# Performance work log

Measured on AMD Instinct MI355X. Metric: run time of the kernel, lower is better.

Reference implementation:

```python
import jax, jax.numpy as jnp
import numpy as np

NUM_LATENT = 1024
LATENT_DIM = 256
BETA = 0.25
N_TOKENS = 65536


def setup_inputs() -> dict:
    key = jax.random.key(0)
    k1, k2 = jax.random.split(key)
    latent_embedding = jax.random.normal(k1, (N_TOKENS, LATENT_DIM), dtype=jnp.float32)
    # torch.nn.init.uniform_(codebook, -1/num_latent, 1/num_latent)
    codebook = jax.random.uniform(
        k2, (NUM_LATENT, LATENT_DIM), dtype=jnp.float32,
        minval=-1.0 / NUM_LATENT, maxval=1.0 / NUM_LATENT)
    return {"latent_embedding": latent_embedding, "codebook": codebook}


def reference(latent_embedding, codebook):
    le_det = jax.lax.stop_gradient(latent_embedding)  # [N, D]
    # distances[n,k] = ||z_n||^2 + ||c_k||^2 - 2 z_n . c_k   (z detached, codebook NOT)
    distances = (jnp.sum(le_det ** 2, axis=1, keepdims=True)
                 + jnp.sum(codebook ** 2, axis=1)
                 - 2.0 * jnp.matmul(le_det, codebook.T))  # [N, K]
    encoding_inds = jnp.argmin(distances, axis=1)  # [N]
    # one_hot @ codebook == gather rows of codebook
    quantized_latents = codebook[encoding_inds]  # [N, D]
    num_latent = codebook.shape[0]
    commitment_loss = jnp.mean((jax.lax.stop_gradient(quantized_latents)
                                - latent_embedding) ** 2) * num_latent
    embedding_loss = jnp.mean((quantized_latents - le_det) ** 2) * num_latent
    vq_loss = embedding_loss + commitment_loss * BETA
    probs = jax.nn.softmax(-distances, axis=1)  # [N, K]
    probs = jnp.clip(jnp.mean(probs, axis=0, keepdims=True), 0.001, 0.999)  # [1, K]
    return (quantized_latents, codebook, probs, vq_loss)
```

## Files before the change

### kernel.cpp

```cpp
#include <hip/hip_runtime.h>

#define N_TOK 65536
#define DIM   256
#define K_CODES 1024
#define CB_OFF    16777216
#define PROBS_OFF (16777216 + 262144)
#define LOSS_OFF  (16777216 + 262144 + 1024)
#define TM 64

typedef float  f32x4  __attribute__((ext_vector_type(4)));
typedef short  s16x8  __attribute__((ext_vector_type(8)));

__device__ __forceinline__ unsigned short f32_to_bf16(float x) {
    unsigned u = __float_as_uint(x);
    unsigned r = (u + 0x7FFFu + ((u >> 16) & 1u)) >> 16;
    return (unsigned short)r;
}
__device__ __forceinline__ unsigned fkey(float a) {
    unsigned u = __float_as_uint(a);
    unsigned m = (unsigned)(((int)u) >> 31);
    return u ^ (m | 0x80000000u);
}
__device__ __forceinline__ float fkey_inv(unsigned k) {
    unsigned u = (k & 0x80000000u) ? (k ^ 0x80000000u) : ~k;
    return __uint_as_float(u);
}

__device__ __forceinline__ unsigned red16_max_u(unsigned v) {
    unsigned t;
    t = (unsigned)__builtin_amdgcn_update_dpp(0, (int)v, 0xB1,  0xF, 0xF, true); v = v > t ? v : t;
    t = (unsigned)__builtin_amdgcn_update_dpp(0, (int)v, 0x4E,  0xF, 0xF, true); v = v > t ? v : t;
    t = (unsigned)__builtin_amdgcn_update_dpp(0, (int)v, 0x141, 0xF, 0xF, true); v = v > t ? v : t;
    t = (unsigned)__builtin_amdgcn_update_dpp(0, (int)v, 0x140, 0xF, 0xF, true); v = v > t ? v : t;
    return v;
}
__device__ __forceinline__ float red16_sum_f(float v) {
    float t;
    t = __uint_as_float((unsigned)__builtin_amdgcn_update_dpp(0, (int)__float_as_uint(v), 0xB1,  0xF, 0xF, true)); v += t;
    t = __uint_as_float((unsigned)__builtin_amdgcn_update_dpp(0, (int)__float_as_uint(v), 0x4E,  0xF, 0xF, true)); v += t;
    t = __uint_as_float((unsigned)__builtin_amdgcn_update_dpp(0, (int)__float_as_uint(v), 0x141, 0xF, 0xF, true)); v += t;
    t = __uint_as_float((unsigned)__builtin_amdgcn_update_dpp(0, (int)__float_as_uint(v), 0x140, 0xF, 0xF, true)); v += t;
    return v;
}

__global__ __launch_bounds__(512) void k_prep(const float* __restrict__ cb,
                                              float* __restrict__ c2,
                                              unsigned short* __restrict__ cbf,
                                              float* __restrict__ probs_part,
                                              float* __restrict__ lossR,
                                              float* __restrict__ outcb,
                                              int zcount, int nloss, int docopy) {
    const int g  = blockIdx.x;
    const int t  = threadIdx.x;
    const int wv = t >> 6;
    const int ln = t & 63;
    const int l15 = ln & 15, q = ln >> 4;

    const float* zp = cb + (size_t)(g * 16 + l15) * DIM + wv * 32 + q * 8;
    f32x4 z0 = *(const f32x4*)(zp);
    f32x4 z1 = *(const f32x4*)(zp + 4);
    s16x8 a;
    a[0] = (short)f32_to_bf16(z0[0]); a[1] = (short)f32_to_bf16(z0[1]);
    a[2] = (short)f32_to_bf16(z0[2]); a[3] = (short)f32_to_bf16(z0[3]);
    a[4] = (short)f32_to_bf16(z1[0]); a[5] = (short)f32_to_bf16(z1[1]);
    a[6] = (short)f32_to_bf16(z1[2]); a[7] = (short)f32_to_bf16(z1[3]);
    *(s16x8*)(cbf + (size_t)(g * 8 + wv) * 1024 + ln * 8) = a;

    float s = z0[0]*z0[0] + z0[1]*z0[1] + z0[2]*z0[2] + z0[3]*z0[3]
            + z1[0]*z1[0] + z1[1]*z1[1] + z1[2]*z1[2] + z1[3]*z1[3];
    s += __shfl_xor(s, 16, 64);
    s += __shfl_xor(s, 32, 64);
    __shared__ float c2p[8][16];
    if (q == 0) c2p[wv][l15] = s;

    const int base = g * 512 + t;
    if (base < nloss) lossR[base] = 0.f;
    if (base < zcount) probs_part[base] = 0.f;
    if (base + 32768 < zcount) probs_part[base + 32768] = 0.f;
    if (docopy) {
        #pragma unroll
        for (int i = 0; i < 8; i++) outcb[base + i * 32768] = cb[base + i * 32768];
    }

    __syncthreads();
    if (t < 16) {
        float acc = 0.f;
        #pragma unroll
        for (int ww = 0; ww < 8; ww++) acc += c2p[ww][t];
        c2[g * 16 + t] = acc;
    }
}

__global__ __launch_bounds__(1024, 4) void k_main(const float* __restrict__ z,
                                                  const float* __restrict__ cb,
                                                  const unsigned short* __restrict__ cbf,
                                                  const float* __restrict__ c2,
                                                  float* __restrict__ out_q,
                                                  float* __restrict__ probs_part,
                                                  float* __restrict__ lossR,
                                                  int repmask) {
    const int t   = threadIdx.x;
    const int w   = t >> 6;
    const int ln  = t & 63;
    const int q   = ln >> 4;
    const int l15 = ln & 15;
    const int k0  = w * 64;
    const int n0  = blockIdx.x * TM;
    float* pp = probs_part +
        (size_t)((repmask < 0) ? (int)blockIdx.x : (int)(blockIdx.x & repmask)) * K_CODES;

    __shared__ unsigned short a_lds[32 * 64 * 8];
    __shared__ float    z2p[32][16];
    __shared__ unsigned kred[16][64];
    __shared__ float    ered[16][64];
    __shared__ int   fidx[64];
    __shared__ float fU[64];

    #pragma unroll
    for (int rep = 0; rep < 2; rep++) {
        const int f   = t + rep * 1024;
        const int md  = w + rep * 16;
        const int m   = md >> 3;
        const int dsv = md & 7;
        const int row = m * 16 + l15;
        const int dim = dsv * 32 + q * 8;
        const float* zp = z + (size_t)(n0 + row) * DIM + dim;
        f32x4 z0 = *(const f32x4*)(zp);
        f32x4 z1 = *(const f32x4*)(zp + 4);
        s16x8 a;
        a[0] = (short)f32_to_bf16(z0[0]); a[1] = (short)f32_to_bf16(z0[1]);
        a[2] = (short)f32_to_bf16(z0[2]); a[3] = (short)f32_to_bf16(z0[3]);
        a[4] = (short)f32_to_bf16(z1[0]); a[5] = (short)f32_to_bf16(z1[1]);
        a[6] = (short)f32_to_bf16(z1[2]); a[7] = (short)f32_to_bf16(z1[3]);
        *(s16x8*)(a_lds + (size_t)f * 8) = a;
        float s = z0[0]*z0[0] + z0[1]*z0[1] + z0[2]*z0[2] + z0[3]*z0[3]
                + z1[0]*z1[0] + z1[1]*z1[1] + z1[2]*z1[2] + z1[3]*z1[3];
        s += __shfl_xor(s, 16, 64);
        s += __shfl_xor(s, 32, 64);
        if (q == 0) z2p[md][l15] = s;
    }

    float c2v[4];
    #pragma unroll
    for (int nt = 0; nt < 4; nt++) c2v[nt] = c2[k0 + nt * 16 + l15];
    f32x4 acc[4][4];
    #pragma unroll
    for (int m = 0; m < 4; m++)
        #pragma unroll
        for (int nt = 0; nt < 4; nt++) {
            const float iv = -0.5f * c2v[nt];
            f32x4 v4 = {iv, iv, iv, iv};
            acc[m][nt] = v4;
        }

    __syncthreads();

    const unsigned short* bb = cbf + (size_t)(w * 4) * 8 * 1024 + ln * 8;
    #pragma unroll
    for (int ds = 0; ds < 8; ds++) {
        s16x8 af[4];
        #pragma unroll
        for (int m = 0; m < 4; m++)
            af[m] = *(const s16x8*)(a_lds + (size_t)((m * 8 + ds) * 64 + ln) * 8);
        #pragma unroll
        for (int nt = 0; nt < 4; nt++) {
            s16x8 b = *(const s16x8*)(bb + (size_t)(nt * 8 + ds) * 1024);
            #pragma unroll
            for (int m = 0; m < 4; m++)
                acc[m][nt] = __builtin_amdgcn_mfma_f32_16x16x32_bf16(af[m], b, acc[m][nt], 0, 0, 0);
        }
    }

    unsigned lkey[4][4];
    float    lesum[4][4];
    #pragma unroll
    for (int m = 0; m < 4; m++)
        #pragma unroll
        for (int v = 0; v < 4; v++) { lkey[m][v] = 0u; lesum[m][v] = 0.f; }

    #pragma unroll
    for (int m = 0; m < 4; m++)
        #pragma unroll
        for (int nt = 0; nt < 4; nt++) {
            const unsigned colc = 1023u - (unsigned)(k0 + nt * 16 + l15);
            #pragma unroll
            for (int v = 0; v < 4; v++) {
                float a = acc[m][nt][v];
                unsigned key = (fkey(a) & 0xFFFFFC00u) | colc;
                lkey[m][v] = max(lkey[m][v], key);
                float e = __expf(a + a);
                acc[m][nt][v] = e;
                lesum[m][v] += e;
            }
        }

    #pragma unroll
    for (int m = 0; m < 4; m++)
        #pragma unroll
        for (int v = 0; v < 4; v++) {
            lkey[m][v]  = red16_max_u(lkey[m][v]);
            lesum[m][v] = red16_sum_f(lesum[m][v]);
        }

    if (l15 == 0) {
        #pragma unroll
        for (int m = 0; m < 4; m++)
            #pragma unroll
            for (int v = 0; v < 4; v++) {
                const int r = m * 16 + q * 4 + v;
                kred[w][r] = lkey[m][v]; ered[w][r] = lesum[m][v];
            }
    }
    __syncthreads();
    float lossreg = 0.f;
    if (t < 64) {
        unsigned bk = kred[0][t];
        float U = ered[0][t];
        #pragma unroll
        for (int ww = 1; ww < 16; ww++) {
            bk = max(bk, kred[ww][t]);
            U += ered[ww][t];
        }
        fidx[t] = 1023 - (int)(bk & 1023u);
        fU[t] = U;
        float a_rec = fkey_inv(bk);
        float z2 = 0.f;
        #pragma unroll
        for (int ds = 0; ds < 8; ds++) z2 += z2p[(t >> 4) * 8 + ds][t & 15];
        lossreg = z2 - 2.0f * a_rec;
    }
    __syncthreads();

    float ps[4];
    #pragma unroll
    for (int nt = 0; nt < 4; nt++) ps[nt] = 0.f;
    #pragma unroll
    for (int m = 0; m < 4; m++)
        #pragma unroll
        for (int v = 0; v < 4; v++) {
            const float invU = 1.0f / fU[m * 16 + q * 4 + v];
            #pragma unroll
            for (int nt = 0; nt < 4; nt++) ps[nt] += acc[m][nt][v] * invU;
        }
    #pragma unroll
    for (int nt = 0; nt < 4; nt++) {
        ps[nt] += __shfl_xor(ps[nt], 16, 64);
        ps[nt] += __shfl_xor(ps[nt], 32, 64);
    }
    if (repmask < 0) pp[k0 + q * 16 + l15] = ps[q];
    else             atomicAdd(&pp[k0 + q * 16 + l15], ps[q]);

    #pragma unroll
    for (int i = 0; i < 4; i++) {
        const int r  = w * 4 + i;
        const int am = fidx[r];
        f32x4 qv = *(const f32x4*)(cb + (size_t)am * DIM + ln * 4);
        *(f32x4*)(out_q + (size_t)(n0 + r) * DIM + ln * 4) = qv;
    }

    if (w == 0) {
        #pragma unroll
        for (int off = 32; off; off >>= 1) lossreg += __shfl_down(lossreg, off, 64);
        if (ln == 0) atomicAdd(&lossR[blockIdx.x & 63], lossreg);
    }
}

__global__ __launch_bounds__(256) void k_fin(const float* __restrict__ cb,
                                             const float* __restrict__ probs_part,
                                             const float* __restrict__ lossR,
                                             float* __restrict__ out,
                                             int R, int nLoss, int docopy) {
    const int g = blockIdx.x * 256 + threadIdx.x;
    __shared__ float part[4][64];
    if (docopy && g < 262144) out[CB_OFF + g] = cb[g];
    if (R == 1024) {
        if (blockIdx.x < 16) {
            const int col   = blockIdx.x * 64 + (threadIdx.x & 63);
            const int chunk = threadIdx.x >> 6;
            const float* p0 = probs_part + (size_t)chunk * 256 * K_CODES + col;
            float a0 = 0.f, a1 = 0.f, a2 = 0.f, a3 = 0.f;
            for (int r = 0; r < 256; r += 4) {
                a0 += p0[(size_t)(r + 0) * K_CODES];
                a1 += p0[(size_t)(r + 1) * K_CODES];
                a2 += p0[(size_t)(r + 2) * K_CODES];
                a3 += p0[(size_t)(r + 3) * K_CODES];
            }
            part[chunk][threadIdx.x & 63] = a0 + a1 + a2 + a3;
            __syncthreads();
            if (threadIdx.x < 64) {
                float p = (part[0][threadIdx.x] + part[1][threadIdx.x]
                         + part[2][threadIdx.x] + part[3][threadIdx.x]) * (1.0f / 65536.0f);
                p = fminf(fmaxf(p, 0.001f), 0.999f);
                out[PROBS_OFF + blockIdx.x * 64 + threadIdx.x] = p;
            }
        }
    } else if (g < K_CODES) {
        float a0 = 0.f, a1 = 0.f, a2 = 0.f, a3 = 0.f;
        if (R >= 4) {
            for (int r = 0; r < R; r += 4) {
                a0 += probs_part[(r + 0) * K_CODES + g];
                a1 += probs_part[(r + 1) * K_CODES + g];
                a2 += probs_part[(r + 2) * K_CODES + g];
                a3 += probs_part[(r + 3) * K_CODES + g];
            }
        } else {
            for (int r = 0; r < R; r++) a0 += probs_part[r * K_CODES + g];
        }
        float p = (a0 + a1 + a2 + a3) * (1.0f / 65536.0f);
        p = fminf(fmaxf(p, 0.001f), 0.999f);
        out[PROBS_OFF + g] = p;
    }
    if (g == 0) {
        float ls = 0.f;
        for (int r = 0; r < nLoss; r++) ls += lossR[r];
        out[LOSS_OFF] = ls * (1280.0f / 16777216.0f);
    }
}

extern "C" void kernel_launch(void* const* d_in, const int* in_sizes, int n_in,
                              void* d_out, int out_size, void* d_ws, size_t ws_size,
                              hipStream_t stream) {
    (void)in_sizes; (void)n_in; (void)out_size;
    const float* z  = (const float*)d_in[0];
    const float* cb = (const float*)d_in[1];
    float* out = (float*)d_out;

    float* c2 = (float*)d_ws;

    float *probs_part, *lossR;
    int R, nLoss, repmask;
    size_t used = 1024 * 4;
    auto fits = [&](int r) { return ws_size >= used + (size_t)(64 + r * 1024) * 4; };
    if      (fits(1024)) R = 1024;
    else if (fits(64))   R = 64;
    else if (fits(16))   R = 16;
    else if (fits(4))    R = 4;
    else                 R = 0;
    const int storeMode = (R == 1024);
    if (R) {
        lossR      = c2 + 1024;
        probs_part = lossR + 64;
        nLoss = 64;
        used += (size_t)(64 + R * 1024) * 4;
        repmask = storeMode ? -1 : (R - 1);
    } else {
        probs_part = out + PROBS_OFF;
        lossR      = out + LOSS_OFF;
        R = 1; nLoss = 1; repmask = 0;
    }

    unsigned short* cbf;
    int cbf_in_ws = (ws_size >= used + (size_t)K_CODES * DIM * 2);
    if (cbf_in_ws) cbf = (unsigned short*)((char*)d_ws + used);
    else           cbf = (unsigned short*)(out + CB_OFF);

    k_prep<<<dim3(64), dim3(512), 0, stream>>>(cb, c2, cbf, probs_part, lossR,
                                               out + CB_OFF, storeMode ? 0 : R * 1024,
                                               nLoss, cbf_in_ws);
    k_main<<<dim3(N_TOK / TM), dim3(1024), 0, stream>>>(z, cb, cbf, c2, out, probs_part,
                                                        lossR, repmask);
    const int fin_blocks = cbf_in_ws ? (storeMode ? 16 : 4) : 1024;
    k_fin<<<dim3(fin_blocks), dim3(256), 0, stream>>>(cb, probs_part, lossR, out,
                                                      R, nLoss, !cbf_in_ws);
}
```

Before: 217.5 us.

## Halve token tile per block and widen per-wave codebook slice

```diff
diff --git a/kernel.cpp b/kernel.cpp
--- a/kernel.cpp
+++ b/kernel.cpp
@@ -6,7 +6,8 @@
 #define CB_OFF    16777216
 #define PROBS_OFF (16777216 + 262144)
 #define LOSS_OFF  (16777216 + 262144 + 1024)
-#define TM 64
+#define TM 32
+#define NBLK (N_TOK / TM)
 
 typedef float  f32x4  __attribute__((ext_vector_type(4)));
 typedef short  s16x8  __attribute__((ext_vector_type(8)));
@@ -64,7 +65,7 @@
     a[2] = (short)f32_to_bf16(z0[2]); a[3] = (short)f32_to_bf16(z0[3]);
     a[4] = (short)f32_to_bf16(z1[0]); a[5] = (short)f32_to_bf16(z1[1]);
     a[6] = (short)f32_to_bf16(z1[2]); a[7] = (short)f32_to_bf16(z1[3]);
-    *(s16x8*)(cbf + (size_t)(g * 8 + wv) * 1024 + ln * 8) = a;
+    *(s16x8*)(cbf + (size_t)(g * 8 + wv) * 512 + ln * 8) = a;
 
     float s = z0[0]*z0[0] + z0[1]*z0[1] + z0[2]*z0[2] + z0[3]*z0[3]
             + z1[0]*z1[0] + z1[1]*z1[1] + z1[2]*z1[2] + z1[3]*z1[3];
@@ -75,8 +76,12 @@
 
     const int base = g * 512 + t;
     if (base < nloss) lossR[base] = 0.f;
-    if (base < zcount) probs_part[base] = 0.f;
-    if (base + 32768 < zcount) probs_part[base + 32768] = 0.f;
+    if (zcount >= 0) {
+        if (base < zcount) probs_part[base] = 0.f;
+        if (base + 32768 < zcount) probs_part[base + 32768] = 0.f;
+    } else {
+        if (base < -zcount) probs_part[(size_t)base * 1024] = 0.f;
+    }
     if (docopy) {
         #pragma unroll
         for (int i = 0; i < 8; i++) outcb[base + i * 32768] = cb[base + i * 32768];
@@ -91,35 +96,34 @@
     }
 }
 
-__global__ __launch_bounds__(1024, 4) void k_main(const float* __restrict__ z,
-                                                  const float* __restrict__ cb,
-                                                  const unsigned short* __restrict__ cbf,
-                                                  const float* __restrict__ c2,
-                                                  float* __restrict__ out_q,
-                                                  float* __restrict__ probs_part,
-                                                  float* __restrict__ lossR,
-                                                  int repmask) {
+__global__ __launch_bounds__(512, 4) void k_main(const float* __restrict__ z,
+                                                 const float* __restrict__ cb,
+                                                 const unsigned short* __restrict__ cbf,
+                                                 const float* __restrict__ c2,
+                                                 float* __restrict__ out_q,
+                                                 float* __restrict__ probs_part,
+                                                 float* __restrict__ lossR,
+                                                 int repmask) {
     const int t   = threadIdx.x;
     const int w   = t >> 6;
     const int ln  = t & 63;
     const int q   = ln >> 4;
     const int l15 = ln & 15;
-    const int k0  = w * 64;
+    const int k0  = w * 128;
     const int n0  = blockIdx.x * TM;
     float* pp = probs_part +
         (size_t)((repmask < 0) ? (int)blockIdx.x : (int)(blockIdx.x & repmask)) * K_CODES;
 
-    __shared__ unsigned short a_lds[32 * 64 * 8];
-    __shared__ float    z2p[32][16];
-    __shared__ unsigned kred[16][64];
-    __shared__ float    ered[16][64];
-    __shared__ int   fidx[64];
-    __shared__ float fU[64];
+    __shared__ unsigned short a_lds[16 * 64 * 8];
+    __shared__ float    z2p[16][16];
+    __shared__ unsigned kred[8][32];
+    __shared__ float    ered[8][32];
+    __shared__ int   fidx[32];
+    __shared__ float fU[32];
 
     #pragma unroll
     for (int rep = 0; rep < 2; rep++) {
-        const int f   = t + rep * 1024;
-        const int md  = w + rep * 16;
+        const int md  = w + rep * 8;
         const int m   = md >> 3;
         const int dsv = md & 7;
         const int row = m * 16 + l15;
@@ -132,7 +136,7 @@
         a[2] = (short)f32_to_bf16(z0[2]); a[3] = (short)f32_to_bf16(z0[3]);
         a[4] = (short)f32_to_bf16(z1[0]); a[5] = (short)f32_to_bf16(z1[1]);
         a[6] = (short)f32_to_bf16(z1[2]); a[7] = (short)f32_to_bf16(z1[3]);
-        *(s16x8*)(a_lds + (size_t)f * 8) = a;
+        *(s16x8*)(a_lds + (size_t)(md * 64 + ln) * 8) = a;
         float s = z0[0]*z0[0] + z0[1]*z0[1] + z0[2]*z0[2] + z0[3]*z0[3]
                 + z1[0]*z1[0] + z1[1]*z1[1] + z1[2]*z1[2] + z1[3]*z1[3];
         s += __shfl_xor(s, 16, 64);
@@ -140,14 +144,14 @@
         if (q == 0) z2p[md][l15] = s;
     }
 
-    float c2v[4];
-    #pragma unroll
-    for (int nt = 0; nt < 4; nt++) c2v[nt] = c2[k0 + nt * 16 + l15];
-    f32x4 acc[4][4];
-    #pragma unroll
-    for (int m = 0; m < 4; m++)
-        #pragma unroll
-        for (int nt = 0; nt < 4; nt++) {
+    float c2v[8];
+    #pragma unroll
+    for (int nt = 0; nt < 8; nt++) c2v[nt] = c2[k0 + nt * 16 + l15];
+    f32x4 acc[2][8];
+    #pragma unroll
+    for (int m = 0; m < 2; m++)
+        #pragma unroll
+        for (int nt = 0; nt < 8; nt++) {
             const float iv = -0.5f * c2v[nt];
             f32x4 v4 = {iv, iv, iv, iv};
             acc[m][nt] = v4;
@@ -155,33 +159,32 @@
 
     __syncthreads();
 
-    const unsigned short* bb = cbf + (size_t)(w * 4) * 8 * 1024 + ln * 8;
+    const unsigned short* bb = cbf + (size_t)(w * 8) * 8 * 512 + ln * 8;
     #pragma unroll
     for (int ds = 0; ds < 8; ds++) {
-        s16x8 af[4];
-        #pragma unroll
-        for (int m = 0; m < 4; m++)
+        s16x8 af[2];
+        #pragma unroll
+        for (int m = 0; m < 2; m++)
             af[m] = *(const s16x8*)(a_lds + (size_t)((m * 8 + ds) * 64 + ln) * 8);
         #pragma unroll
-        for (int nt = 0; nt < 4; nt++) {
-            s16x8 b = *(const s16x8*)(bb + (size_t)(nt * 8 + ds) * 1024);
-            #pragma unroll
-            for (int m = 0; m < 4; m++)
-                acc[m][nt] = __builtin_amdgcn_mfma_f32_16x16x32_bf16(af[m], b, acc[m][nt], 0, 0, 0);
-        }
-    }
-
-    unsigned lkey[4][4];
-    float    lesum[4][4];
-    #pragma unroll
-    for (int m = 0; m < 4; m++)
+        for (int nt = 0; nt < 8; nt++) {
+            s16x8 b = *(const s16x8*)(bb + (size_t)(nt * 8 + ds) * 512);
+            acc[0][nt] = __builtin_amdgcn_mfma_f32_16x16x32_bf16(af[0], b, acc[0][nt], 0, 0, 0);
+            acc[1][nt] = __builtin_amdgcn_mfma_f32_16x16x32_bf16(af[1], b, acc[1][nt], 0, 0, 0);
+        }
+    }
+
+    unsigned lkey[2][4];
+    float    lesum[2][4];
+    #pragma unroll
+    for (int m = 0; m < 2; m++)
         #pragma unroll
         for (int v = 0; v < 4; v++) { lkey[m][v] = 0u; lesum[m][v] = 0.f; }
 
     #pragma unroll
-    for (int m = 0; m < 4; m++)
-        #pragma unroll
-        for (int nt = 0; nt < 4; nt++) {
+    for (int m = 0; m < 2; m++)
+        #pragma unroll
+        for (int nt = 0; nt < 8; nt++) {
             const unsigned colc = 1023u - (unsigned)(k0 + nt * 16 + l15);
             #pragma unroll
             for (int v = 0; v < 4; v++) {
@@ -195,7 +198,7 @@
         }
 
     #pragma unroll
-    for (int m = 0; m < 4; m++)
+    for (int m = 0; m < 2; m++)
         #pragma unroll
         for (int v = 0; v < 4; v++) {
             lkey[m][v]  = red16_max_u(lkey[m][v]);
@@ -204,7 +207,7 @@
 
     if (l15 == 0) {
         #pragma unroll
-        for (int m = 0; m < 4; m++)
+        for (int m = 0; m < 2; m++)
             #pragma unroll
             for (int v = 0; v < 4; v++) {
                 const int r = m * 16 + q * 4 + v;
@@ -213,11 +216,11 @@
     }
     __syncthreads();
     float lossreg = 0.f;
-    if (t < 64) {
+    if (t < 32) {
         unsigned bk = kred[0][t];
         float U = ered[0][t];
         #pragma unroll
-        for (int ww = 1; ww < 16; ww++) {
+        for (int ww = 1; ww < 8; ww++) {
             bk = max(bk, kred[ww][t]);
             U += ered[ww][t];
         }
@@ -231,24 +234,28 @@
     }
     __syncthreads();
 
-    float ps[4];
-    #pragma unroll
-    for (int nt = 0; nt < 4; nt++) ps[nt] = 0.f;
-    #pragma unroll
-    for (int m = 0; m < 4; m++)
+    float ps[8];
+    #pragma unroll
+    for (int nt = 0; nt < 8; nt++) ps[nt] = 0.f;
+    #pragma unroll
+    for (int m = 0; m < 2; m++)
         #pragma unroll
         for (int v = 0; v < 4; v++) {
             const float invU = 1.0f / fU[m * 16 + q * 4 + v];
             #pragma unroll
-            for (int nt = 0; nt < 4; nt++) ps[nt] += acc[m][nt][v] * invU;
-        }
-    #pragma unroll
-    for (int nt = 0; nt < 4; nt++) {
+            for (int nt = 0; nt < 8; nt++) ps[nt] += acc[m][nt][v] * invU;
+        }
+    #pragma unroll
+    for (int nt = 0; nt < 8; nt++) {
         ps[nt] += __shfl_xor(ps[nt], 16, 64);
         ps[nt] += __shfl_xor(ps[nt], 32, 64);
     }
-    if (repmask < 0) pp[k0 + q * 16 + l15] = ps[q];
-    else             atomicAdd(&pp[k0 + q * 16 + l15], ps[q]);
+    #pragma unroll
+    for (int h = 0; h < 2; h++) {
+        const int nt = q * 2 + h;
+        if (repmask < 0) pp[k0 + nt * 16 + l15] = ps[nt];
+        else             atomicAdd(&pp[k0 + nt * 16 + l15], ps[nt]);
+    }
 
     #pragma unroll
     for (int i = 0; i < 4; i++) {
@@ -273,13 +280,14 @@
     const int g = blockIdx.x * 256 + threadIdx.x;
     __shared__ float part[4][64];
     if (docopy && g < 262144) out[CB_OFF + g] = cb[g];
-    if (R == 1024) {
+    if (R >= 1024) {
         if (blockIdx.x < 16) {
             const int col   = blockIdx.x * 64 + (threadIdx.x & 63);
             const int chunk = threadIdx.x >> 6;
-            const float* p0 = probs_part + (size_t)chunk * 256 * K_CODES + col;
+            const int rows  = R >> 2;
+            const float* p0 = probs_part + (size_t)chunk * rows * K_CODES + col;
             float a0 = 0.f, a1 = 0.f, a2 = 0.f, a3 = 0.f;
-            for (int r = 0; r < 256; r += 4) {
+            for (int r = 0; r < rows; r += 4) {
                 a0 += p0[(size_t)(r + 0) * K_CODES];
                 a1 += p0[(size_t)(r + 1) * K_CODES];
                 a2 += p0[(size_t)(r + 2) * K_CODES];
@@ -331,17 +339,17 @@
     int R, nLoss, repmask;
     size_t used = 1024 * 4;
     auto fits = [&](int r) { return ws_size >= used + (size_t)(64 + r * 1024) * 4; };
-    if      (fits(1024)) R = 1024;
+    if      (fits(NBLK)) R = NBLK;
     else if (fits(64))   R = 64;
     else if (fits(16))   R = 16;
     else if (fits(4))    R = 4;
     else                 R = 0;
-    const int storeMode = (R == 1024);
+    const int storeMode = (R == NBLK);
     if (R) {
         lossR      = c2 + 1024;
         probs_part = lossR + 64;
         nLoss = 64;
-        used += (size_t)(64 + R * 1024) * 4;
+        used += (size_t)(64 + (size_t)R * 1024) * 4;
         repmask = storeMode ? -1 : (R - 1);
     } else {
         probs_part = out + PROBS_OFF;
@@ -355,11 +363,11 @@
     else           cbf = (unsigned short*)(out + CB_OFF);
 
     k_prep<<<dim3(64), dim3(512), 0, stream>>>(cb, c2, cbf, probs_part, lossR,
-                                               out + CB_OFF, storeMode ? 0 : R * 1024,
+                                               out + CB_OFF, storeMode ? -NBLK : R * 1024,
                                                nLoss, cbf_in_ws);
-    k_main<<<dim3(N_TOK / TM), dim3(1024), 0, stream>>>(z, cb, cbf, c2, out, probs_part,
-                                                        lossR, repmask);
-    const int fin_blocks = cbf_in_ws ? (storeMode ? 16 : 4) : 1024;
+    k_main<<<dim3(NBLK), dim3(512), 0, stream>>>(z, cb, cbf, c2, out, probs_part,
+                                                 lossR, repmask);
+    const int fin_blocks = (!cbf_in_ws) ? 1024 : (storeMode ? 16 : 4);
     k_fin<<<dim3(fin_blocks), dim3(256), 0, stream>>>(cb, probs_part, lossR, out,
                                                       R, nLoss, !cbf_in_ws);
 }
```

Measured after the change: 234.9 us. +8.0%, slower.
